# Kernel optimization log

Hardware: AMD Instinct MI355X
Metric: run time of the kernel (lower is better)

The kernel has to match this reference:

```python
import jax, jax.numpy as jnp
import numpy as np

NEG_SLOPE = 0.2  # PyG GATConv default negative_slope
EPS = 1e-16     # PyG softmax denominator epsilon


def gat_layer(x, src, dst, W, att_src, att_dst, bias, N):
    """PyG-style GATConv: gather -> leaky-relu score -> segment softmax -> scatter-add.
    x: [N, F_in], W: [F_in, H*C], att_src/att_dst: [H, C], bias: [H*C].
    src/dst: [E] edge endpoints (messages flow src -> dst), self-loops included.
    """
    H, C = att_src.shape
    h = (x @ W).reshape(N, H, C)                       # [N, H, C]
    a_s = jnp.sum(h * att_src, axis=-1)                # [N, H]
    a_d = jnp.sum(h * att_dst, axis=-1)                # [N, H]
    e = a_s[src] + a_d[dst]                            # [E, H]
    e = jnp.where(e > 0, e, NEG_SLOPE * e)             # leaky relu
    m = jax.ops.segment_max(e, dst, num_segments=N)    # [N, H] (self-loops ensure every node hit)
    p = jnp.exp(e - m[dst])                            # [E, H]
    s = jax.ops.segment_sum(p, dst, num_segments=N)    # [N, H]
    alpha = p / (s[dst] + EPS)                         # [E, H]
    out = jax.ops.segment_sum(alpha[:, :, None] * h[src], dst, num_segments=N)  # [N, H, C]
    return out.reshape(N, H * C) + bias


def setup_inputs() -> dict:
    key = jax.random.key(0)
    ks = jax.random.split(key, 12)
    N, E = 100000, 1600000
    x = jax.random.normal(ks[0], (N, 1), dtype=jnp.float32)
    edge_index = jax.random.randint(ks[1], (2, E), 0, N, dtype=jnp.int32)
    sc = 0.1
    # conv1: in=1, heads=4, out=8
    W1 = jax.random.normal(ks[2], (1, 32), dtype=jnp.float32) * sc
    att_src1 = jax.random.normal(ks[3], (4, 8), dtype=jnp.float32) * sc
    att_dst1 = jax.random.normal(ks[4], (4, 8), dtype=jnp.float32) * sc
    bias1 = jnp.zeros((32,), dtype=jnp.float32)
    # conv2: in=32, heads=8, out=8
    W2 = jax.random.normal(ks[5], (32, 64), dtype=jnp.float32) * sc
    att_src2 = jax.random.normal(ks[6], (8, 8), dtype=jnp.float32) * sc
    att_dst2 = jax.random.normal(ks[7], (8, 8), dtype=jnp.float32) * sc
    bias2 = jnp.zeros((64,), dtype=jnp.float32)
    # fc2: 64 -> 1
    fc_w = jax.random.normal(ks[8], (64, 1), dtype=jnp.float32) * sc
    fc_b = jnp.zeros((1,), dtype=jnp.float32)
    return {"x": x, "edge_index": edge_index,
            "W1": W1, "att_src1": att_src1, "att_dst1": att_dst1, "bias1": bias1,
            "W2": W2, "att_src2": att_src2, "att_dst2": att_dst2, "bias2": bias2,
            "fc_w": fc_w, "fc_b": fc_b}


def reference(x, edge_index, W1, att_src1, att_dst1, bias1,
              W2, att_src2, att_dst2, bias2, fc_w, fc_b):
    N = x.shape[0]
    loop = jnp.arange(N, dtype=edge_index.dtype)       # add_self_loops=True (PyG default)
    src = jnp.concatenate([edge_index[0], loop])
    dst = jnp.concatenate([edge_index[1], loop])
    h = jax.nn.elu(gat_layer(x, src, dst, W1, att_src1, att_dst1, bias1, N))
    h = jax.nn.elu(gat_layer(h, src, dst, W2, att_src2, att_dst2, bias2, N))
    return h @ fc_w + fc_b                             # [N, 1]
```

## Files before the change

kernel.cpp:

```cpp
#include <hip/hip_runtime.h>
#include <hip/hip_fp16.h>
#include <cmath>

#define TPB 256
#define NSLOPE 0.2f
#define SEPS 1e-16f

#define BSH 7
#define BNODES 128
#define NBMAX 1024
#define NCHUNK 256
#define SCTPB 1024
#define SCSTAGE 6720
#define STAGE 2816
#define MAXDEG 96

__device__ __forceinline__ float lrelu(float v) { return v > 0.f ? v : NSLOPE * v; }
__device__ __forceinline__ float elu1(float v)  { return v > 0.f ? v : expm1f(v); }
__device__ __forceinline__ float elu1f(float v) { return v > 0.f ? v : __expf(v) - 1.f; }

__global__ void k_prep(const float* __restrict__ W1, const float* __restrict__ as1,
                       const float* __restrict__ ad1, float* __restrict__ SD,
                       unsigned* __restrict__ bucketCursor, int NB, unsigned cap) {
    int t = threadIdx.x;
    for (int i = t; i < NB; i += blockDim.x) bucketCursor[(size_t)i * 16] = (unsigned)i * cap;
    if (t < 8) {
        int h = t & 3;
        const float* att = (t >= 4) ? ad1 : as1;
        float acc = 0.f;
        #pragma unroll
        for (int c = 0; c < 8; ++c) acc += W1[h*8+c] * att[h*8+c];
        SD[t] = acc;
    }
}

__global__ void k_bscatter(const int* __restrict__ srcI, const int* __restrict__ dstI,
                           int E, int N, int NB, int chunk,
                           unsigned* __restrict__ bucketCursor, int* __restrict__ pk) {
    __shared__ int cnt[NBMAX];
    __shared__ unsigned base[NBMAX];
    __shared__ int offl[NBMAX];
    __shared__ int rval[SCSTAGE];
    __shared__ unsigned short rbkt[SCSTAGE];
    __shared__ int wtot[16], woff[16];
    int t = threadIdx.x;
    int lane = t & 63, wv = t >> 6;
    int ET = E + N;
    int beg = blockIdx.x * chunk;
    int end = min(beg + chunk, ET);
    int m = end - beg;
    for (int i = t; i < NBMAX; i += blockDim.x) cnt[i] = 0;
    __syncthreads();
    for (int e = beg + t; e < end; e += blockDim.x) {
        int d = (e < E) ? dstI[e] : (e - E);
        atomicAdd(&cnt[d >> BSH], 1);
    }
    __syncthreads();
    int v = cnt[t];
    int inc = v;
    #pragma unroll
    for (int off = 1; off < 64; off <<= 1) {
        int u = __shfl_up(inc, off);
        if (lane >= off) inc += u;
    }
    if (lane == 63) wtot[wv] = inc;
    __syncthreads();
    if (t < 16) {
        int xv = wtot[t];
        int sc_ = xv;
        #pragma unroll
        for (int off = 1; off < 16; off <<= 1) {
            int u = __shfl_up(sc_, off);
            if (t >= off) sc_ += u;
        }
        woff[t] = sc_ - xv;
    }
    __syncthreads();
    offl[t] = inc + woff[wv] - v;
    if (t < NB) {
        base[t] = v ? atomicAdd(&bucketCursor[(size_t)t * 16], (unsigned)v) : 0u;
        cnt[t] = 0;
    }
    __syncthreads();
    if (m <= SCSTAGE) {
        for (int e = beg + t; e < end; e += blockDim.x) {
            int s, d;
            if (e < E) { s = srcI[e]; d = dstI[e]; } else { s = d = e - E; }
            int b = d >> BSH;
            int r = atomicAdd(&cnt[b], 1);
            int slot = offl[b] + r;
            rval[slot] = (s << BSH) | (d & (BNODES - 1));
            rbkt[slot] = (unsigned short)b;
        }
        __syncthreads();
        for (int slot = t; slot < m; slot += blockDim.x) {
            int b = rbkt[slot];
            pk[base[b] + (unsigned)(slot - offl[b])] = rval[slot];
        }
    } else {
        for (int e = beg + t; e < end; e += blockDim.x) {
            int s, d;
            if (e < E) { s = srcI[e]; d = dstI[e]; } else { s = d = e - E; }
            int b = d >> BSH;
            int r = atomicAdd(&cnt[b], 1);
            pk[base[b] + (unsigned)r] = (s << BSH) | (d & (BNODES - 1));
        }
    }
}

__global__ void k_sl1h2(const int* __restrict__ pk, const unsigned* __restrict__ bucketCursor,
                        unsigned cap,
                        const float* __restrict__ x, const float* __restrict__ SD,
                        const float* __restrict__ W1, const float* __restrict__ b1,
                        const float* __restrict__ W2, const float* __restrict__ attS,
                        const float* __restrict__ attD, int N,
                        unsigned* __restrict__ offsets, int* __restrict__ sortedSrc,
                        __half* __restrict__ h2h, float* __restrict__ aS, float* __restrict__ aD) {
    __shared__ __align__(16) char upool[BNODES * 36 * 4];
    int* praw = (int*)upool;
    float (*lds1)[36] = (float (*)[36])upool;
    __shared__ int sorted[STAGE];
    __shared__ int cnt[BNODES];
    __shared__ int offl[BNODES];
    __shared__ int w0tot;
    int b = blockIdx.x, t = threadIdx.x;
    unsigned rbeg = (unsigned)b * cap;
    int m = (int)(bucketCursor[(size_t)b * 16] - rbeg);
    bool inLds = (m <= STAGE);
    int base = b << BSH;
    if (t < BNODES) cnt[t] = 0;
    __syncthreads();
    if (inLds) {
        for (int i = t; i < m; i += TPB) {
            int p = pk[rbeg + i];
            praw[i] = p;
            atomicAdd(&cnt[p & (BNODES - 1)], 1);
        }
    } else {
        for (int i = t; i < m; i += TPB) atomicAdd(&cnt[pk[rbeg + i] & (BNODES - 1)], 1);
    }
    __syncthreads();
    int v = (t < BNODES) ? cnt[t] : 0;
    int inc = v;
    #pragma unroll
    for (int off = 1; off < 64; off <<= 1) {
        int u = __shfl_up(inc, off);
        if ((t & 63) >= off) inc += u;
    }
    if (t == 63) w0tot = inc;
    __syncthreads();
    if (t >= 64 && t < BNODES) inc += w0tot;
    if (t < BNODES) {
        int ex = inc - v;
        int d = base + t;
        if (d < N) offsets[d] = ((rbeg + (unsigned)ex) << 10) | (unsigned)v;
        cnt[t] = 0;
        offl[t] = ex;
    }
    __syncthreads();
    if (inLds) {
        for (int i = t; i < m; i += TPB) {
            int p = praw[i];
            int dl = p & (BNODES - 1);
            int r = atomicAdd(&cnt[dl], 1);
            sorted[offl[dl] + r] = p >> BSH;
        }
        __syncthreads();
        for (int i = t; i < m; i += TPB) sortedSrc[rbeg + i] = sorted[i];
    } else {
        for (int i = t; i < m; i += TPB) {
            int p = pk[rbeg + i];
            int dl = p & (BNODES - 1);
            int r = atomicAdd(&cnt[dl], 1);
            sortedSrc[rbeg + (unsigned)(offl[dl] + r)] = p >> BSH;
        }
        __syncthreads();
    }
    __syncthreads();
    int n = t >> 1, half = t & 1;
    int d2 = base + n;
    bool active = (d2 < N);
    float s0 = 0.f, s1 = 0.f, s2 = 0.f, s3 = 0.f;
    float g0 = 0.f, g1 = 0.f, g2 = 0.f, g3 = 0.f;
    if (active) {
        int deg = cnt[n];
        int lbeg = offl[n];
        float xd = x[d2];
        float S0 = SD[0], S1 = SD[1], S2 = SD[2], S3 = SD[3];
        float D0 = xd*SD[4], D1 = xd*SD[5], D2 = xd*SD[6], D3 = xd*SD[7];
        int dh = (deg + 1) >> 1;
        int i = lbeg + (half ? dh : 0);
        int rem = half ? (deg - dh) : dh;
        for (; rem >= 2; rem -= 2, i += 2) {
            int a0 = inLds ? sorted[i]   : sortedSrc[rbeg + i];
            int a1 = inLds ? sorted[i+1] : sortedSrc[rbeg + i + 1];
            float x0 = x[a0], x1 = x[a1];
            float p;
            p = __expf(lrelu(x0*S0 + D0)); s0 += p; g0 += p * x0;
            p = __expf(lrelu(x0*S1 + D1)); s1 += p; g1 += p * x0;
            p = __expf(lrelu(x0*S2 + D2)); s2 += p; g2 += p * x0;
            p = __expf(lrelu(x0*S3 + D3)); s3 += p; g3 += p * x0;
            p = __expf(lrelu(x1*S0 + D0)); s0 += p; g0 += p * x1;
            p = __expf(lrelu(x1*S1 + D1)); s1 += p; g1 += p * x1;
            p = __expf(lrelu(x1*S2 + D2)); s2 += p; g2 += p * x1;
            p = __expf(lrelu(x1*S3 + D3)); s3 += p; g3 += p * x1;
        }
        if (rem > 0) {
            int a0 = inLds ? sorted[i] : sortedSrc[rbeg + i];
            float xs = x[a0];
            float p;
            p = __expf(lrelu(xs*S0 + D0)); s0 += p; g0 += p * xs;
            p = __expf(lrelu(xs*S1 + D1)); s1 += p; g1 += p * xs;
            p = __expf(lrelu(xs*S2 + D2)); s2 += p; g2 += p * xs;
            p = __expf(lrelu(xs*S3 + D3)); s3 += p; g3 += p * xs;
        }
    }
    s0 += __shfl_xor(s0, 1); s1 += __shfl_xor(s1, 1);
    s2 += __shfl_xor(s2, 1); s3 += __shfl_xor(s3, 1);
    g0 += __shfl_xor(g0, 1); g1 += __shfl_xor(g1, 1);
    g2 += __shfl_xor(g2, 1); g3 += __shfl_xor(g3, 1);
    if (active) {
        float gg[4];
        gg[0] = g0 / (s0 + SEPS); gg[1] = g1 / (s1 + SEPS);
        gg[2] = g2 / (s2 + SEPS); gg[3] = g3 / (s3 + SEPS);
        int h0 = half * 2;
        #pragma unroll
        for (int hh = 0; hh < 2; ++hh)
            #pragma unroll
            for (int cc = 0; cc < 8; ++cc)
                lds1[n][(h0+hh)*8+cc] = elu1(gg[h0+hh] * W1[(h0+hh)*8+cc] + b1[(h0+hh)*8+cc]);
    }
    __syncthreads();
    int lane = t & 63;
    int sub = t >> 6;
    float w2r[32];
    #pragma unroll
    for (int k = 0; k < 32; ++k) w2r[k] = W2[k*64 + lane];
    float attSl = attS[lane], attDl = attD[lane];
    int nCnt = min(BNODES, N - base);
    for (int nn = sub; nn < nCnt; nn += 4) {
        const float4* row4 = (const float4*)lds1[nn];
        float acc = 0.f;
        #pragma unroll
        for (int k4 = 0; k4 < 8; ++k4) {
            float4 rv = row4[k4];
            acc += rv.x*w2r[4*k4] + rv.y*w2r[4*k4+1] + rv.z*w2r[4*k4+2] + rv.w*w2r[4*k4+3];
        }
        int node = base + nn;
        h2h[(size_t)node*64 + lane] = __float2half(acc);
        float ps = acc * attSl;
        float pd = acc * attDl;
        #pragma unroll
        for (int mm = 1; mm < 8; mm <<= 1) {
            ps += __shfl_xor(ps, mm);
            pd += __shfl_xor(pd, mm);
        }
        int hh = lane >> 3, cc = lane & 7;
        if (cc == 0) aS[(size_t)node*8 + hh] = ps;
        if (cc == 1) aD[(size_t)node*8 + hh] = pd;
    }
}

__global__ void k_agg(const unsigned* __restrict__ offsets, const int* __restrict__ ss,
                      const float* __restrict__ aS, const float* __restrict__ aD,
                      const __half* __restrict__ h2h, const float* __restrict__ b2,
                      const float* __restrict__ fcw, const float* __restrict__ fcb,
                      float* __restrict__ out, int N) {
    __shared__ int sl[4][MAXDEG];
    int lane = threadIdx.x & 63;
    int w = threadIdx.x >> 6;
    int d = blockIdx.x * 4 + w;
    if (d >= N) return;
    unsigned u = offsets[d];
    unsigned beg = u >> 10;
    int deg = (int)(u & 1023u);
    int lH   = lane & 31;
    int half = lane >> 5;
    int hh   = lH >> 2;
    const __half2* __restrict__ hp = (const __half2*)h2h;
    float sum = 0.f, ax = 0.f, ay = 0.f;
    if (deg <= MAXDEG) {
        int degPad = (deg + 7) & ~7;
        for (int j = lane; j < degPad; j += 64) sl[w][j] = ss[beg + (unsigned)min(j, deg - 1)];
        float adv = aD[(unsigned)d * 8u + (unsigned)hh];
        for (int e = 0; e < degPad; e += 8) {
            int bi = e + half;
            int s0 = sl[w][bi],     s1 = sl[w][bi + 2];
            int s2 = sl[w][bi + 4], s3 = sl[w][bi + 6];
            float a0 = aS[(unsigned)s0 * 8u + (unsigned)hh];
            float a1 = aS[(unsigned)s1 * 8u + (unsigned)hh];
            float a2 = aS[(unsigned)s2 * 8u + (unsigned)hh];
            float a3 = aS[(unsigned)s3 * 8u + (unsigned)hh];
            float2 g0 = __half22float2(hp[(unsigned)s0 * 32u + (unsigned)lH]);
            float2 g1 = __half22float2(hp[(unsigned)s1 * 32u + (unsigned)lH]);
            float2 g2 = __half22float2(hp[(unsigned)s2 * 32u + (unsigned)lH]);
            float2 g3 = __half22float2(hp[(unsigned)s3 * 32u + (unsigned)lH]);
            float p0 = __expf(lrelu(a0 + adv));
            float p1 = __expf(lrelu(a1 + adv));
            float p2 = __expf(lrelu(a2 + adv));
            float p3 = __expf(lrelu(a3 + adv));
            if (e + 8 > deg) {
                if (bi     >= deg) p0 = 0.f;
                if (bi + 2 >= deg) p1 = 0.f;
                if (bi + 4 >= deg) p2 = 0.f;
                if (bi + 6 >= deg) p3 = 0.f;
            }
            ax += p0*g0.x + p1*g1.x + p2*g2.x + p3*g3.x;
            ay += p0*g0.y + p1*g1.y + p2*g2.y + p3*g3.y;
            sum += (p0 + p1) + (p2 + p3);
        }
    } else {
        float adh = aD[(size_t)d*8 + hh];
        for (int e = half; e < deg; e += 2) {
            int s = ss[beg + e];
            float p = __expf(lrelu(aS[(size_t)s*8 + hh] + adh));
            float2 g = __half22float2(*(const __half2*)(h2h + (size_t)s*64 + 2*lH));
            ax += p*g.x; ay += p*g.y; sum += p;
        }
    }
    ax  += __shfl_xor(ax, 32);
    ay  += __shfl_xor(ay, 32);
    sum += __shfl_xor(sum, 32);
    float inv = 1.f / (sum + SEPS);
    float tt = elu1f(ax*inv + b2[2*lH]) * fcw[2*lH]
             + elu1f(ay*inv + b2[2*lH+1]) * fcw[2*lH+1];
    #pragma unroll
    for (int m = 16; m; m >>= 1) tt += __shfl_xor(tt, m);
    if (lane == 0) out[d] = tt + fcb[0];
}

extern "C" void kernel_launch(void* const* d_in, const int* in_sizes, int n_in,
                              void* d_out, int out_size, void* d_ws, size_t ws_size,
                              hipStream_t stream) {
    const float* x    = (const float*)d_in[0];
    const int*   ei   = (const int*)  d_in[1];
    const float* W1   = (const float*)d_in[2];
    const float* as1  = (const float*)d_in[3];
    const float* ad1  = (const float*)d_in[4];
    const float* b1   = (const float*)d_in[5];
    const float* W2   = (const float*)d_in[6];
    const float* attS2= (const float*)d_in[7];
    const float* attD2= (const float*)d_in[8];
    const float* b2   = (const float*)d_in[9];
    const float* fcw  = (const float*)d_in[10];
    const float* fcb  = (const float*)d_in[11];
    float* out = (float*)d_out;

    int N = in_sizes[0];
    int E = in_sizes[1] / 2;
    int ET = E + N;
    int NB = (N + BNODES - 1) / BNODES;
    unsigned cap = (unsigned)((ET + NB - 1) / NB + 512);
    cap = (cap + 3u) & ~3u;
    size_t padded = (size_t)NB * cap;

    const int* srcI = ei;
    const int* dstI = ei + E;

    float* ws = (float*)d_ws;
    size_t off = 0;
    float*    SD           = ws + off; off += 16;
    unsigned* bucketCursor = (unsigned*)(ws + off); off += (size_t)NBMAX * 16;
    unsigned* offsets      = (unsigned*)(ws + off); off += (size_t)N + 16;
    int*      pk           = (int*)(ws + off); off += padded;
    int*      sortedSrc    = (int*)(ws + off); off += padded;
    float*    aS2          = ws + off; off += (size_t)N * 8;
    float*    aD2          = ws + off; off += (size_t)N * 8;
    __half*   h2h          = (__half*)(ws + off); off += (size_t)N * 32;

    k_prep<<<1, 1024, 0, stream>>>(W1, as1, ad1, SD, bucketCursor, NB, cap);

    int chunk = (ET + NCHUNK - 1) / NCHUNK;
    k_bscatter<<<NCHUNK, SCTPB, 0, stream>>>(srcI, dstI, E, N, NB, chunk, bucketCursor, pk);
    k_sl1h2   <<<NB, TPB, 0, stream>>>(pk, bucketCursor, cap, x, SD, W1, b1, W2, attS2, attD2,
                                       N, offsets, sortedSrc, h2h, aS2, aD2);
    k_agg     <<<(N + 3) / 4, TPB, 0, stream>>>(offsets, sortedSrc, aS2, aD2, h2h,
                                                b2, fcw, fcb, out, N);
}
```

Before: 193.5 us.

## Split final GAT aggregation into two head-half passes to shrink gather working set

The final aggregation kernel is templated on a head offset and launched twice, each pass handling four of the eight heads with four edges processed concurrently per warp. The first pass writes a partial fc projection to a temporary buffer and the second adds it and the bias. This is meant to halve the per-pass footprint of gathered half-precision features and attention scores to improve cache hit rates. In exchange, edge indices and offsets are read twice, an extra launch is added, and each gather fetches narrower row segments.

```diff
diff --git a/kernel.cpp b/kernel.cpp
--- a/kernel.cpp
+++ b/kernel.cpp
@@ -261,11 +261,13 @@
     }
 }
 
-__global__ void k_agg(const unsigned* __restrict__ offsets, const int* __restrict__ ss,
-                      const float* __restrict__ aS, const float* __restrict__ aD,
-                      const __half* __restrict__ h2h, const float* __restrict__ b2,
-                      const float* __restrict__ fcw, const float* __restrict__ fcb,
-                      float* __restrict__ out, int N) {
+template<int HB>
+__global__ void k_aggh(const unsigned* __restrict__ offsets, const int* __restrict__ ss,
+                       const float* __restrict__ aS, const float* __restrict__ aD,
+                       const __half* __restrict__ h2h, const float* __restrict__ b2,
+                       const float* __restrict__ fcw, const float* __restrict__ fcb,
+                       const float* __restrict__ tmpIn, float* __restrict__ tmpOut,
+                       float* __restrict__ out, int N) {
     __shared__ int sl[4][MAXDEG];
     int lane = threadIdx.x & 63;
     int w = threadIdx.x >> 6;
@@ -274,59 +276,47 @@
     unsigned u = offsets[d];
     unsigned beg = u >> 10;
     int deg = (int)(u & 1023u);
-    int lH   = lane & 31;
-    int half = lane >> 5;
-    int hh   = lH >> 2;
+    int lH4 = lane & 15;
+    int q   = lane >> 4;
+    int h4  = lH4 >> 2;
     const __half2* __restrict__ hp = (const __half2*)h2h;
     float sum = 0.f, ax = 0.f, ay = 0.f;
+    float adv = aD[(unsigned)d * 8u + (unsigned)(HB + h4)];
     if (deg <= MAXDEG) {
-        int degPad = (deg + 7) & ~7;
+        int degPad = (deg + 3) & ~3;
         for (int j = lane; j < degPad; j += 64) sl[w][j] = ss[beg + (unsigned)min(j, deg - 1)];
-        float adv = aD[(unsigned)d * 8u + (unsigned)hh];
-        for (int e = 0; e < degPad; e += 8) {
-            int bi = e + half;
-            int s0 = sl[w][bi],     s1 = sl[w][bi + 2];
-            int s2 = sl[w][bi + 4], s3 = sl[w][bi + 6];
-            float a0 = aS[(unsigned)s0 * 8u + (unsigned)hh];
-            float a1 = aS[(unsigned)s1 * 8u + (unsigned)hh];
-            float a2 = aS[(unsigned)s2 * 8u + (unsigned)hh];
-            float a3 = aS[(unsigned)s3 * 8u + (unsigned)hh];
-            float2 g0 = __half22float2(hp[(unsigned)s0 * 32u + (unsigned)lH]);
-            float2 g1 = __half22float2(hp[(unsigned)s1 * 32u + (unsigned)lH]);
-            float2 g2 = __half22float2(hp[(unsigned)s2 * 32u + (unsigned)lH]);
-            float2 g3 = __half22float2(hp[(unsigned)s3 * 32u + (unsigned)lH]);
-            float p0 = __expf(lrelu(a0 + adv));
-            float p1 = __expf(lrelu(a1 + adv));
-            float p2 = __expf(lrelu(a2 + adv));
-            float p3 = __expf(lrelu(a3 + adv));
-            if (e + 8 > deg) {
-                if (bi     >= deg) p0 = 0.f;
-                if (bi + 2 >= deg) p1 = 0.f;
-                if (bi + 4 >= deg) p2 = 0.f;
-                if (bi + 6 >= deg) p3 = 0.f;
+        for (int e = 0; e < degPad; e += 4) {
+            int bi = e + q;
+            int s = sl[w][bi];
+            float a = aS[(unsigned)s * 8u + (unsigned)(HB + h4)];
+            float2 g = __half22float2(hp[(unsigned)s * 32u + (unsigned)(HB * 4 + lH4)]);
+            float p = __expf(lrelu(a + adv));
+            if (e + 4 > deg) {
+                if (bi >= deg) p = 0.f;
             }
-            ax += p0*g0.x + p1*g1.x + p2*g2.x + p3*g3.x;
-            ay += p0*g0.y + p1*g1.y + p2*g2.y + p3*g3.y;
-            sum += (p0 + p1) + (p2 + p3);
+            ax += p * g.x; ay += p * g.y; sum += p;
         }
     } else {
-        float adh = aD[(size_t)d*8 + hh];
-        for (int e = half; e < deg; e += 2) {
+        for (int e = q; e < deg; e += 4) {
             int s = ss[beg + e];
-            float p = __expf(lrelu(aS[(size_t)s*8 + hh] + adh));
-            float2 g = __half22float2(*(const __half2*)(h2h + (size_t)s*64 + 2*lH));
-            ax += p*g.x; ay += p*g.y; sum += p;
-        }
-    }
-    ax  += __shfl_xor(ax, 32);
-    ay  += __shfl_xor(ay, 32);
-    sum += __shfl_xor(sum, 32);
+            float p = __expf(lrelu(aS[(unsigned)s * 8u + (unsigned)(HB + h4)] + adv));
+            float2 g = __half22float2(hp[(unsigned)s * 32u + (unsigned)(HB * 4 + lH4)]);
+            ax += p * g.x; ay += p * g.y; sum += p;
+        }
+    }
+    ax  += __shfl_xor(ax, 16);  ax  += __shfl_xor(ax, 32);
+    ay  += __shfl_xor(ay, 16);  ay  += __shfl_xor(ay, 32);
+    sum += __shfl_xor(sum, 16); sum += __shfl_xor(sum, 32);
     float inv = 1.f / (sum + SEPS);
-    float tt = elu1f(ax*inv + b2[2*lH]) * fcw[2*lH]
-             + elu1f(ay*inv + b2[2*lH+1]) * fcw[2*lH+1];
+    int c0 = HB * 8 + 2 * lH4;
+    float tt = elu1f(ax * inv + b2[c0])     * fcw[c0]
+             + elu1f(ay * inv + b2[c0 + 1]) * fcw[c0 + 1];
     #pragma unroll
-    for (int m = 16; m; m >>= 1) tt += __shfl_xor(tt, m);
-    if (lane == 0) out[d] = tt + fcb[0];
+    for (int m = 8; m; m >>= 1) tt += __shfl_xor(tt, m);
+    if (lane == 0) {
+        if (HB == 0) tmpOut[d] = tt;
+        else         out[d] = tt + tmpIn[d] + fcb[0];
+    }
 }
 
 extern "C" void kernel_launch(void* const* d_in, const int* in_sizes, int n_in,
@@ -366,7 +356,9 @@
     int*      sortedSrc    = (int*)(ws + off); off += padded;
     float*    aS2          = ws + off; off += (size_t)N * 8;
     float*    aD2          = ws + off; off += (size_t)N * 8;
+    off = (off + 31) & ~(size_t)31;
     __half*   h2h          = (__half*)(ws + off); off += (size_t)N * 32;
+    float*    tmp          = ws + off; off += (size_t)N;
 
     k_prep<<<1, 1024, 0, stream>>>(W1, as1, ad1, SD, bucketCursor, NB, cap);
 
@@ -374,6 +366,8 @@
     k_bscatter<<<NCHUNK, SCTPB, 0, stream>>>(srcI, dstI, E, N, NB, chunk, bucketCursor, pk);
     k_sl1h2   <<<NB, TPB, 0, stream>>>(pk, bucketCursor, cap, x, SD, W1, b1, W2, attS2, attD2,
                                        N, offsets, sortedSrc, h2h, aS2, aD2);
-    k_agg     <<<(N + 3) / 4, TPB, 0, stream>>>(offsets, sortedSrc, aS2, aD2, h2h,
-                                                b2, fcw, fcb, out, N);
-}
+    k_aggh<0> <<<(N + 3) / 4, TPB, 0, stream>>>(offsets, sortedSrc, aS2, aD2, h2h,
+                                                b2, fcw, fcb, nullptr, tmp, nullptr, N);
+    k_aggh<4> <<<(N + 3) / 4, TPB, 0, stream>>>(offsets, sortedSrc, aS2, aD2, h2h,
+                                                b2, fcw, fcb, tmp, nullptr, out, N);
+}
```

After: 236.2 us. 22.1% more time.
